# Kernel tuning notes

Hardware: AMD Instinct MI355X
Metric: run time of the kernel (lower is better)

Reference implementation:

```python
import jax, jax.numpy as jnp
import numpy as np

HK, WK = 7, 11  # local_k


def _local_mask(H, W):
    # Equivalent to the torch buffer: 0 inside the hk x wk window centered on the
    # query position (for odd hk, wk), -inf outside. Shape (N, N), N = H*W.
    n = jnp.arange(H * W)
    hq, wq = n // W, n % W
    dh = jnp.abs(hq[:, None] - hq[None, :])
    dw = jnp.abs(wq[:, None] - wq[None, :])
    allowed = (dh <= HK // 2) & (dw <= WK // 2)
    return jnp.where(allowed, 0.0, -jnp.inf).astype(jnp.float32)


def setup_inputs() -> dict:
    key = jax.random.key(0)
    k1, k2, k3 = jax.random.split(key, 3)
    B, H, W, C = 8, 32, 64, 512
    N = H * W
    x = jax.random.normal(k1, (B, N, C), dtype=jnp.float32)
    qkv_w = jax.random.normal(k2, (3 * C, C), dtype=jnp.float32) * (C ** -0.5)
    proj_w = jax.random.normal(k3, (C, C), dtype=jnp.float32) * (C ** -0.5)
    proj_b = jnp.zeros((C,), dtype=jnp.float32)
    return {"x": x, "qkv_w": qkv_w, "proj_w": proj_w, "proj_b": proj_b, "H": H, "W": W}


def reference(x, qkv_w, proj_w, proj_b, H, W):
    B, N, C = x.shape
    num_heads = 8
    head_dim = C // num_heads
    scale = head_dim ** -0.5

    # qkv: Linear(dim, 3*dim, bias=False) -> (B, N, 3, heads, head_dim)
    qkv = (x @ qkv_w.T).reshape(B, N, 3, num_heads, head_dim)
    q = qkv[:, :, 0].transpose(0, 2, 1, 3) * scale  # (B, h, N, d)
    k = qkv[:, :, 1].transpose(0, 2, 1, 3)
    v = qkv[:, :, 2].transpose(0, 2, 1, 3)

    attn = jnp.einsum('bhnd,bhmd->bhnm', q, k)  # (B, h, N, N)
    attn = attn + _local_mask(H, W)  # broadcast over (B, h)
    attn = jax.nn.softmax(attn, axis=-1)

    out = jnp.einsum('bhnm,bhmd->bhnd', attn, v)  # (B, h, N, d)
    out = out.transpose(0, 2, 1, 3).reshape(B, N, C)
    return out @ proj_w.T + proj_b
```

## Files before the change

kernel.cpp:

```cpp
#include <hip/hip_runtime.h>
#include <hip/hip_bf16.h>

#define B_SZ 8
#define H_SZ 32
#define W_SZ 64
#define N_SZ 2048
#define C_SZ 512
#define NH 8
#define HD 64

using u16 = unsigned short;
typedef __attribute__((ext_vector_type(8))) short s16x8;
typedef __attribute__((ext_vector_type(4))) float f32x4;

__device__ __forceinline__ float bf2f(u16 u) {
    union { unsigned int i; float f; } c; c.i = ((unsigned int)u) << 16; return c.f;
}
__device__ __forceinline__ u16 f2bf(float f) {
    union { float f; unsigned int i; } c; c.f = f;
    unsigned int r = c.i + 0x7fffu + ((c.i >> 16) & 1u);
    return (u16)(r >> 16);
}

#define GLL16(gp, lp) __builtin_amdgcn_global_load_lds( \
    (const __attribute__((address_space(1))) unsigned int*)(gp), \
    (__attribute__((address_space(3))) unsigned int*)(lp), 16, 0, 0)

__global__ __launch_bounds__(256) void conv_f2b(const float* __restrict__ in,
                                                u16* __restrict__ out, int n4) {
    int i = blockIdx.x * 256 + threadIdx.x;
    if (i < n4) {
        float4 v = ((const float4*)in)[i];
        ushort4 o = { f2bf(v.x), f2bf(v.y), f2bf(v.z), f2bf(v.w) };
        ((ushort4*)out)[i] = o;
    }
}
__global__ __launch_bounds__(256) void conv_qkvw(const float* __restrict__ in,
                                                 u16* __restrict__ out) {
    int i = blockIdx.x * 256 + threadIdx.x;
    float4 v = ((const float4*)in)[i];
    const float sc = (i < (512 * 512 / 4)) ? 0.125f : 1.0f;
    ushort4 o = { f2bf(v.x * sc), f2bf(v.y * sc), f2bf(v.z * sc), f2bf(v.w * sc) };
    ((ushort4*)out)[i] = o;
}

template<int MODE>
__global__ __launch_bounds__(256)
void gemm_mfma(const u16* __restrict__ A, const u16* __restrict__ Bw,
               const float* __restrict__ bias,
               u16* __restrict__ q_ws, u16* __restrict__ k_ws, u16* __restrict__ v_ws,
               float* __restrict__ outp, int K)
{
    __shared__ u16 As[128 * 32];
    __shared__ u16 Bs[128 * 32];
    const int t    = threadIdx.x;
    const int m0   = blockIdx.x * 128;
    const int n0   = blockIdx.y * 128;
    const int wave = t >> 6, lane = t & 63;
    const int wm   = (wave >> 1) << 6;
    const int wn   = (wave & 1) << 6;
    const int l16  = lane & 15, quad = lane >> 4;
    const int srow = t >> 2;
    const int soff = (t & 3) << 3;

    f32x4 acc[4][4] = {};

    for (int k0 = 0; k0 < K; k0 += 32) {
        __syncthreads();
        GLL16(A  + (size_t)(m0 + srow)      * K + k0 + soff, &As[t * 8]);
        GLL16(A  + (size_t)(m0 + 64 + srow) * K + k0 + soff, &As[t * 8 + 2048]);
        GLL16(Bw + (size_t)(n0 + srow)      * K + k0 + soff, &Bs[t * 8]);
        GLL16(Bw + (size_t)(n0 + 64 + srow) * K + k0 + soff, &Bs[t * 8 + 2048]);
        __syncthreads();

        s16x8 af[4], bf[4];
        #pragma unroll
        for (int i = 0; i < 4; ++i)
            af[i] = *(const s16x8*)&As[(wm + 16 * i + l16) * 32 + quad * 8];
        #pragma unroll
        for (int j = 0; j < 4; ++j)
            bf[j] = *(const s16x8*)&Bs[(wn + 16 * j + l16) * 32 + quad * 8];
        #pragma unroll
        for (int i = 0; i < 4; ++i)
            #pragma unroll
            for (int j = 0; j < 4; ++j)
                acc[i][j] = __builtin_amdgcn_mfma_f32_16x16x32_bf16(af[i], bf[j], acc[i][j], 0, 0, 0);
    }

    #pragma unroll
    for (int i = 0; i < 4; ++i) {
        #pragma unroll
        for (int j = 0; j < 4; ++j) {
            const int gn = n0 + wn + 16 * j + l16;
            #pragma unroll
            for (int r = 0; r < 4; ++r) {
                const int gm = m0 + wm + 16 * i + quad * 4 + r;
                const float val = acc[i][j][r];
                if (MODE == 0) {
                    const int bb = gm >> 11, nn = gm & 2047;
                    const int s = gn >> 9, rem = gn & 511;
                    const int h = rem >> 6, dd = rem & 63;
                    if (s == 0)
                        q_ws[((((size_t)bb * NH + h) * N_SZ) + nn) * HD + dd] = f2bf(val);
                    else if (s == 1)
                        k_ws[((((size_t)bb * NH + h) * N_SZ) + nn) * HD + dd] = f2bf(val);
                    else
                        v_ws[((((size_t)bb * NH + h) * HD) + dd) * N_SZ + nn] = f2bf(val);
                } else {
                    outp[(size_t)gm * C_SZ + gn] = val + bias[gn];
                }
            }
        }
    }
}

__global__ __launch_bounds__(256)
void attn_mfma(const u16* __restrict__ q_ws, const u16* __restrict__ k_ws,
               const u16* __restrict__ vt_ws, u16* __restrict__ o_ws)
{
    __shared__ u16 Qs[64 * 64];
    __shared__ u16 Ks[64 * 64];
    __shared__ u16 Vt[64 * 64];
    __shared__ u16 Ps[4][16 * 72];

    const int t = threadIdx.x, wave = t >> 6, lane = t & 63;
    const int l16 = lane & 15, quad = lane >> 4;
    const int u  = blockIdx.x;
    const int hq = u & 31;
    const int bh = u >> 5;
    const size_t base = (size_t)bh * (N_SZ * HD);

    const u16* qg = q_ws + base + (size_t)hq * (64 * HD);
    GLL16(qg + t * 8,        &Qs[t * 8]);
    GLL16(qg + t * 8 + 2048, &Qs[t * 8 + 2048]);
    __syncthreads();

    s16x8 aQ0 = *(const s16x8*)&Qs[(16 * wave + l16) * 64 + quad * 8];
    s16x8 aQ1 = *(const s16x8*)&Qs[(16 * wave + l16) * 64 + 32 + quad * 8];

    f32x4 accO[4] = {};
    float lp[4] = {0.f, 0.f, 0.f, 0.f};

    const int h0 = (hq - 3 < 0) ? 0 : hq - 3;
    const int h1 = (hq + 3 > H_SZ - 1) ? H_SZ - 1 : hq + 3;

    for (int hh = h0; hh <= h1; ++hh) {
        __syncthreads();
        const u16* kg = k_ws + base + (size_t)hh * (64 * HD);
        GLL16(kg + t * 8,        &Ks[t * 8]);
        GLL16(kg + t * 8 + 2048, &Ks[t * 8 + 2048]);
        const u16* vg = vt_ws + base + (size_t)hh * 64;
        GLL16(vg + (size_t)(t >> 3) * N_SZ + ((t & 7) << 3),        &Vt[t * 8]);
        GLL16(vg + (size_t)((t >> 3) + 32) * N_SZ + ((t & 7) << 3), &Vt[t * 8 + 2048]);
        __syncthreads();

        f32x4 sacc[4];
        #pragma unroll
        for (int j = 0; j < 4; ++j) {
            s16x8 b0 = *(const s16x8*)&Ks[(16 * j + l16) * 64 + quad * 8];
            s16x8 b1 = *(const s16x8*)&Ks[(16 * j + l16) * 64 + 32 + quad * 8];
            f32x4 z = {0.f, 0.f, 0.f, 0.f};
            z = __builtin_amdgcn_mfma_f32_16x16x32_bf16(aQ0, b0, z, 0, 0, 0);
            sacc[j] = __builtin_amdgcn_mfma_f32_16x16x32_bf16(aQ1, b1, z, 0, 0, 0);
        }

        const int wq0 = 16 * wave + quad * 4;
        #pragma unroll
        for (int j = 0; j < 4; ++j) {
            const int ww = 16 * j + l16;
            #pragma unroll
            for (int r = 0; r < 4; ++r) {
                const int dw = ww - (wq0 + r);
                const float p = (dw <= 5 && dw >= -5) ? __expf(sacc[j][r]) : 0.f;
                const u16 pb = f2bf(p);
                lp[r] += bf2f(pb);
                Ps[wave][(quad * 4 + r) * 72 + ww] = pb;
            }
        }

        s16x8 aP0 = *(const s16x8*)&Ps[wave][l16 * 72 + quad * 8];
        s16x8 aP1 = *(const s16x8*)&Ps[wave][l16 * 72 + 32 + quad * 8];
        #pragma unroll
        for (int j = 0; j < 4; ++j) {
            s16x8 v0 = *(const s16x8*)&Vt[(16 * j + l16) * 64 + quad * 8];
            s16x8 v1 = *(const s16x8*)&Vt[(16 * j + l16) * 64 + 32 + quad * 8];
            accO[j] = __builtin_amdgcn_mfma_f32_16x16x32_bf16(aP0, v0, accO[j], 0, 0, 0);
            accO[j] = __builtin_amdgcn_mfma_f32_16x16x32_bf16(aP1, v1, accO[j], 0, 0, 0);
        }
    }

    #pragma unroll
    for (int r = 0; r < 4; ++r) {
        lp[r] += __shfl_xor(lp[r], 1);
        lp[r] += __shfl_xor(lp[r], 2);
        lp[r] += __shfl_xor(lp[r], 4);
        lp[r] += __shfl_xor(lp[r], 8);
    }

    const int bb = bh >> 3, h = bh & 7;
    #pragma unroll
    for (int j = 0; j < 4; ++j) {
        #pragma unroll
        for (int r = 0; r < 4; ++r) {
            const int row = hq * 64 + 16 * wave + quad * 4 + r;
            const float val = accO[j][r] / lp[r];
            o_ws[((size_t)bb * N_SZ + row) * C_SZ + h * 64 + 16 * j + l16] = f2bf(val);
        }
    }
}

extern "C" void kernel_launch(void* const* d_in, const int* in_sizes, int n_in,
                              void* d_out, int out_size, void* d_ws, size_t ws_size,
                              hipStream_t stream)
{
    const float* x      = (const float*)d_in[0];
    const float* qkv_w  = (const float*)d_in[1];
    const float* proj_w = (const float*)d_in[2];
    const float* proj_b = (const float*)d_in[3];
    float* outp = (float*)d_out;

    const size_t seg = (size_t)B_SZ * NH * N_SZ * HD;
    u16* q_ws = (u16*)d_ws;
    u16* k_ws = q_ws + seg;
    u16* v_ws = k_ws + seg;
    u16* o_ws = v_ws + seg;
    u16* xb   = o_ws + seg;
    u16* qwb  = xb + (size_t)16384 * 512;
    u16* pwb  = qwb + (size_t)1536 * 512;

    conv_f2b <<<8192, 256, 0, stream>>>(x, xb, 16384 * 512 / 4);
    conv_qkvw<<<768,  256, 0, stream>>>(qkv_w, qwb);
    conv_f2b <<<256,  256, 0, stream>>>(proj_w, pwb, 512 * 512 / 4);

    gemm_mfma<0><<<dim3(128, 12), 256, 0, stream>>>(xb, qwb, nullptr,
                                                    q_ws, k_ws, v_ws, nullptr, C_SZ);
    attn_mfma<<<B_SZ * NH * H_SZ, 256, 0, stream>>>(q_ws, k_ws, v_ws, o_ws);
    gemm_mfma<1><<<dim3(128, 4), 256, 0, stream>>>(o_ws, pwb, proj_b,
                                                   nullptr, nullptr, nullptr, outp, C_SZ);
}
```

Before: 208.0 us.

## Swizzle LDS layouts, widen GEMM K-tile, skip masked key tiles in attention

Adds an XOR-swizzled LDS layout for the GEMM tiles and the attention Q/K/V tiles to reduce bank conflicts, and doubles the GEMM K step to 64. Each attention wave now computes scores for only the 32-column band of keys that can fall inside the 11-wide window, instead of all 64 keys, which halves the QK and PV MFMA work. The QKV GEMM epilogue writes V with vectorized ushort4 stores and hoists the per-segment branching out of the inner loop. The projection GEMM switches to 64-wide N tiles, doubling the grid to 1024 blocks for more parallelism. The changes add index arithmetic and depend on the window fitting inside the chosen 32-key band.

```diff
diff --git a/kernel.cpp b/kernel.cpp
--- a/kernel.cpp
+++ b/kernel.cpp
@@ -26,6 +26,10 @@
     (const __attribute__((address_space(1))) unsigned int*)(gp), \
     (__attribute__((address_space(3))) unsigned int*)(lp), 16, 0, 0)
 
+__device__ __forceinline__ int lds_off(int row, int chunk) {
+    return (row * 8 + (chunk ^ (row & 7))) * 8;
+}
+
 __global__ __launch_bounds__(256) void conv_f2b(const float* __restrict__ in,
                                                 u16* __restrict__ out, int n4) {
     int i = blockIdx.x * 256 + threadIdx.x;
@@ -44,72 +48,103 @@
     ((ushort4*)out)[i] = o;
 }
 
-template<int MODE>
+template<int MODE, int NT>
 __global__ __launch_bounds__(256)
 void gemm_mfma(const u16* __restrict__ A, const u16* __restrict__ Bw,
                const float* __restrict__ bias,
                u16* __restrict__ q_ws, u16* __restrict__ k_ws, u16* __restrict__ v_ws,
                float* __restrict__ outp, int K)
 {
-    __shared__ u16 As[128 * 32];
-    __shared__ u16 Bs[128 * 32];
+    constexpr int NJ = (NT == 128) ? 4 : 2;
+    __shared__ u16 As[128 * 64];
+    __shared__ u16 Bs[NT * 64];
     const int t    = threadIdx.x;
     const int m0   = blockIdx.x * 128;
-    const int n0   = blockIdx.y * 128;
+    const int n0   = blockIdx.y * NT;
     const int wave = t >> 6, lane = t & 63;
     const int wm   = (wave >> 1) << 6;
-    const int wn   = (wave & 1) << 6;
+    const int wn   = (wave & 1) * (NJ * 16);
     const int l16  = lane & 15, quad = lane >> 4;
-    const int srow = t >> 2;
-    const int soff = (t & 3) << 3;
-
-    f32x4 acc[4][4] = {};
-
-    for (int k0 = 0; k0 < K; k0 += 32) {
-        __syncthreads();
-        GLL16(A  + (size_t)(m0 + srow)      * K + k0 + soff, &As[t * 8]);
-        GLL16(A  + (size_t)(m0 + 64 + srow) * K + k0 + soff, &As[t * 8 + 2048]);
-        GLL16(Bw + (size_t)(n0 + srow)      * K + k0 + soff, &Bs[t * 8]);
-        GLL16(Bw + (size_t)(n0 + 64 + srow) * K + k0 + soff, &Bs[t * 8 + 2048]);
-        __syncthreads();
-
-        s16x8 af[4], bf[4];
+    const int srow = t >> 3;
+    const int sch  = (t & 7) ^ (srow & 7);
+
+    f32x4 acc[4][NJ] = {};
+
+    for (int k0 = 0; k0 < K; k0 += 64) {
+        __syncthreads();
+        #pragma unroll
+        for (int g = 0; g < 4; ++g)
+            GLL16(A + (size_t)(m0 + 32 * g + srow) * K + k0 + sch * 8,
+                  &As[g * 2048 + t * 8]);
+        #pragma unroll
+        for (int g = 0; g < NT / 32; ++g)
+            GLL16(Bw + (size_t)(n0 + 32 * g + srow) * K + k0 + sch * 8,
+                  &Bs[g * 2048 + t * 8]);
+        __syncthreads();
+
+        s16x8 af[4][2], bf[NJ][2];
+        #pragma unroll
+        for (int i = 0; i < 4; ++i) {
+            const int R = wm + 16 * i + l16;
+            af[i][0] = *(const s16x8*)&As[lds_off(R, quad)];
+            af[i][1] = *(const s16x8*)&As[lds_off(R, 4 + quad)];
+        }
+        #pragma unroll
+        for (int j = 0; j < NJ; ++j) {
+            const int R = wn + 16 * j + l16;
+            bf[j][0] = *(const s16x8*)&Bs[lds_off(R, quad)];
+            bf[j][1] = *(const s16x8*)&Bs[lds_off(R, 4 + quad)];
+        }
         #pragma unroll
         for (int i = 0; i < 4; ++i)
-            af[i] = *(const s16x8*)&As[(wm + 16 * i + l16) * 32 + quad * 8];
-        #pragma unroll
-        for (int j = 0; j < 4; ++j)
-            bf[j] = *(const s16x8*)&Bs[(wn + 16 * j + l16) * 32 + quad * 8];
-        #pragma unroll
-        for (int i = 0; i < 4; ++i)
-            #pragma unroll
-            for (int j = 0; j < 4; ++j)
-                acc[i][j] = __builtin_amdgcn_mfma_f32_16x16x32_bf16(af[i], bf[j], acc[i][j], 0, 0, 0);
-    }
-
-    #pragma unroll
-    for (int i = 0; i < 4; ++i) {
-        #pragma unroll
-        for (int j = 0; j < 4; ++j) {
+            #pragma unroll
+            for (int j = 0; j < NJ; ++j) {
+                acc[i][j] = __builtin_amdgcn_mfma_f32_16x16x32_bf16(af[i][0], bf[j][0], acc[i][j], 0, 0, 0);
+                acc[i][j] = __builtin_amdgcn_mfma_f32_16x16x32_bf16(af[i][1], bf[j][1], acc[i][j], 0, 0, 0);
+            }
+    }
+
+    if (MODE == 0) {
+        const int bb  = m0 >> 11;
+        const int nnb = (m0 & 2047) + wm + (quad << 2);
+        if (n0 >= 1024) {
+            #pragma unroll
+            for (int j = 0; j < NJ; ++j) {
+                const int c  = n0 - 1024 + wn + 16 * j + l16;
+                const int h  = c >> 6, dd = c & 63;
+                u16* vp = v_ws + (((size_t)bb * NH + h) * HD + dd) * N_SZ + nnb;
+                #pragma unroll
+                for (int i = 0; i < 4; ++i) {
+                    ushort4 st = { f2bf(acc[i][j][0]), f2bf(acc[i][j][1]),
+                                   f2bf(acc[i][j][2]), f2bf(acc[i][j][3]) };
+                    *(ushort4*)(vp + 16 * i) = st;
+                }
+            }
+        } else {
+            u16* T = (n0 < 512) ? q_ws : k_ws;
+            #pragma unroll
+            for (int j = 0; j < NJ; ++j) {
+                const int gn = n0 + wn + 16 * j + l16;
+                const int h  = (gn >> 6) & 7, dd = gn & 63;
+                u16* tp = T + (((size_t)bb * NH + h) * N_SZ + nnb) * HD + dd;
+                #pragma unroll
+                for (int i = 0; i < 4; ++i)
+                    #pragma unroll
+                    for (int r = 0; r < 4; ++r)
+                        tp[(size_t)(16 * i + r) * HD] = f2bf(acc[i][j][r]);
+            }
+        }
+    } else {
+        #pragma unroll
+        for (int j = 0; j < NJ; ++j) {
             const int gn = n0 + wn + 16 * j + l16;
-            #pragma unroll
-            for (int r = 0; r < 4; ++r) {
-                const int gm = m0 + wm + 16 * i + quad * 4 + r;
-                const float val = acc[i][j][r];
-                if (MODE == 0) {
-                    const int bb = gm >> 11, nn = gm & 2047;
-                    const int s = gn >> 9, rem = gn & 511;
-                    const int h = rem >> 6, dd = rem & 63;
-                    if (s == 0)
-                        q_ws[((((size_t)bb * NH + h) * N_SZ) + nn) * HD + dd] = f2bf(val);
-                    else if (s == 1)
-                        k_ws[((((size_t)bb * NH + h) * N_SZ) + nn) * HD + dd] = f2bf(val);
-                    else
-                        v_ws[((((size_t)bb * NH + h) * HD) + dd) * N_SZ + nn] = f2bf(val);
-                } else {
-                    outp[(size_t)gm * C_SZ + gn] = val + bias[gn];
-                }
-            }
+            const float bv = bias[gn];
+            #pragma unroll
+            for (int i = 0; i < 4; ++i)
+                #pragma unroll
+                for (int r = 0; r < 4; ++r)
+                    outp[(size_t)(m0 + wm + 16 * i + (quad << 2) + r) * C_SZ + gn]
+                        = acc[i][j][r] + bv;
         }
     }
 }
@@ -121,7 +156,7 @@
     __shared__ u16 Qs[64 * 64];
     __shared__ u16 Ks[64 * 64];
     __shared__ u16 Vt[64 * 64];
-    __shared__ u16 Ps[4][16 * 72];
+    __shared__ u16 Ps[4][16 * 40];
 
     const int t = threadIdx.x, wave = t >> 6, lane = t & 63;
     const int l16 = lane & 15, quad = lane >> 4;
@@ -129,14 +164,19 @@
     const int hq = u & 31;
     const int bh = u >> 5;
     const size_t base = (size_t)bh * (N_SZ * HD);
+    const int srow = t >> 3;
+    const int sch  = (t & 7) ^ (srow & 7);
 
     const u16* qg = q_ws + base + (size_t)hq * (64 * HD);
-    GLL16(qg + t * 8,        &Qs[t * 8]);
-    GLL16(qg + t * 8 + 2048, &Qs[t * 8 + 2048]);
+    GLL16(qg + (size_t)srow        * 64 + sch * 8, &Qs[t * 8]);
+    GLL16(qg + (size_t)(srow + 32) * 64 + sch * 8, &Qs[2048 + t * 8]);
     __syncthreads();
 
-    s16x8 aQ0 = *(const s16x8*)&Qs[(16 * wave + l16) * 64 + quad * 8];
-    s16x8 aQ1 = *(const s16x8*)&Qs[(16 * wave + l16) * 64 + 32 + quad * 8];
+    const int Rq = 16 * wave + l16;
+    s16x8 aQ0 = *(const s16x8*)&Qs[lds_off(Rq, quad)];
+    s16x8 aQ1 = *(const s16x8*)&Qs[lds_off(Rq, 4 + quad)];
+
+    const int kb = min(max(16 * wave - 8, 0), 32);
 
     f32x4 accO[4] = {};
     float lp[4] = {0.f, 0.f, 0.f, 0.f};
@@ -147,45 +187,38 @@
     for (int hh = h0; hh <= h1; ++hh) {
         __syncthreads();
         const u16* kg = k_ws + base + (size_t)hh * (64 * HD);
-        GLL16(kg + t * 8,        &Ks[t * 8]);
-        GLL16(kg + t * 8 + 2048, &Ks[t * 8 + 2048]);
+        GLL16(kg + (size_t)srow        * 64 + sch * 8, &Ks[t * 8]);
+        GLL16(kg + (size_t)(srow + 32) * 64 + sch * 8, &Ks[2048 + t * 8]);
         const u16* vg = vt_ws + base + (size_t)hh * 64;
-        GLL16(vg + (size_t)(t >> 3) * N_SZ + ((t & 7) << 3),        &Vt[t * 8]);
-        GLL16(vg + (size_t)((t >> 3) + 32) * N_SZ + ((t & 7) << 3), &Vt[t * 8 + 2048]);
-        __syncthreads();
-
-        f32x4 sacc[4];
-        #pragma unroll
-        for (int j = 0; j < 4; ++j) {
-            s16x8 b0 = *(const s16x8*)&Ks[(16 * j + l16) * 64 + quad * 8];
-            s16x8 b1 = *(const s16x8*)&Ks[(16 * j + l16) * 64 + 32 + quad * 8];
+        GLL16(vg + (size_t)srow        * N_SZ + sch * 8, &Vt[t * 8]);
+        GLL16(vg + (size_t)(srow + 32) * N_SZ + sch * 8, &Vt[2048 + t * 8]);
+        __syncthreads();
+
+        #pragma unroll
+        for (int j = 0; j < 2; ++j) {
+            const int Rk = kb + 16 * j + l16;
+            s16x8 b0 = *(const s16x8*)&Ks[lds_off(Rk, quad)];
+            s16x8 b1 = *(const s16x8*)&Ks[lds_off(Rk, 4 + quad)];
             f32x4 z = {0.f, 0.f, 0.f, 0.f};
             z = __builtin_amdgcn_mfma_f32_16x16x32_bf16(aQ0, b0, z, 0, 0, 0);
-            sacc[j] = __builtin_amdgcn_mfma_f32_16x16x32_bf16(aQ1, b1, z, 0, 0, 0);
-        }
-
-        const int wq0 = 16 * wave + quad * 4;
-        #pragma unroll
-        for (int j = 0; j < 4; ++j) {
-            const int ww = 16 * j + l16;
+            z = __builtin_amdgcn_mfma_f32_16x16x32_bf16(aQ1, b1, z, 0, 0, 0);
+            const int ww = kb + 16 * j + l16;
             #pragma unroll
             for (int r = 0; r < 4; ++r) {
-                const int dw = ww - (wq0 + r);
-                const float p = (dw <= 5 && dw >= -5) ? __expf(sacc[j][r]) : 0.f;
+                const int dw = ww - (16 * wave + quad * 4 + r);
+                const float p = (dw * dw <= 25) ? __expf(z[r]) : 0.f;
                 const u16 pb = f2bf(p);
                 lp[r] += bf2f(pb);
-                Ps[wave][(quad * 4 + r) * 72 + ww] = pb;
-            }
-        }
-
-        s16x8 aP0 = *(const s16x8*)&Ps[wave][l16 * 72 + quad * 8];
-        s16x8 aP1 = *(const s16x8*)&Ps[wave][l16 * 72 + 32 + quad * 8];
+                Ps[wave][(quad * 4 + r) * 40 + 16 * j + l16] = pb;
+            }
+        }
+
+        s16x8 aP = *(const s16x8*)&Ps[wave][l16 * 40 + quad * 8];
         #pragma unroll
         for (int j = 0; j < 4; ++j) {
-            s16x8 v0 = *(const s16x8*)&Vt[(16 * j + l16) * 64 + quad * 8];
-            s16x8 v1 = *(const s16x8*)&Vt[(16 * j + l16) * 64 + 32 + quad * 8];
-            accO[j] = __builtin_amdgcn_mfma_f32_16x16x32_bf16(aP0, v0, accO[j], 0, 0, 0);
-            accO[j] = __builtin_amdgcn_mfma_f32_16x16x32_bf16(aP1, v1, accO[j], 0, 0, 0);
+            const int Rv = 16 * j + l16;
+            s16x8 vf = *(const s16x8*)&Vt[lds_off(Rv, (kb >> 3) + quad)];
+            accO[j] = __builtin_amdgcn_mfma_f32_16x16x32_bf16(aP, vf, accO[j], 0, 0, 0);
         }
     }
 
@@ -203,8 +236,8 @@
         #pragma unroll
         for (int r = 0; r < 4; ++r) {
             const int row = hq * 64 + 16 * wave + quad * 4 + r;
-            const float val = accO[j][r] / lp[r];
-            o_ws[((size_t)bb * N_SZ + row) * C_SZ + h * 64 + 16 * j + l16] = f2bf(val);
+            o_ws[((size_t)bb * N_SZ + row) * C_SZ + h * 64 + 16 * j + l16]
+                = f2bf(accO[j][r] / lp[r]);
         }
     }
 }
@@ -232,9 +265,9 @@
     conv_qkvw<<<768,  256, 0, stream>>>(qkv_w, qwb);
     conv_f2b <<<256,  256, 0, stream>>>(proj_w, pwb, 512 * 512 / 4);
 
-    gemm_mfma<0><<<dim3(128, 12), 256, 0, stream>>>(xb, qwb, nullptr,
-                                                    q_ws, k_ws, v_ws, nullptr, C_SZ);
+    gemm_mfma<0, 128><<<dim3(128, 12), 256, 0, stream>>>(xb, qwb, nullptr,
+                                                         q_ws, k_ws, v_ws, nullptr, C_SZ);
     attn_mfma<<<B_SZ * NH * H_SZ, 256, 0, stream>>>(q_ws, k_ws, v_ws, o_ws);
-    gemm_mfma<1><<<dim3(128, 4), 256, 0, stream>>>(o_ws, pwb, proj_b,
-                                                   nullptr, nullptr, nullptr, outp, C_SZ);
-}
+    gemm_mfma<1, 64><<<dim3(128, 8), 256, 0, stream>>>(o_ws, pwb, proj_b,
+                                                       nullptr, nullptr, nullptr, outp, C_SZ);
+}
```

New measurement: 186.3 us. -10.4%, faster.
